# Kernel optimization log

Hardware: AMD Instinct MI355X
Metric: run time of the kernel (lower is better)

## Reference

```python
import jax, jax.numpy as jnp
import numpy as np

ROUTING_ITERS = 3
EPS = 1e-12


def squash(s):
    # squash over both pose-matrix dims (axis=[-2,-1])
    n2 = jnp.sum(s * s, axis=(-2, -1), keepdims=True)
    n = jnp.sqrt(n2 + EPS)
    return s * (n2 / (1.0 + n2)) / n


def setup_inputs() -> dict:
    key = jax.random.key(0)
    k1, k2, k3 = jax.random.split(key, 3)
    B, I, O = 32, 4096, 32
    input_poses = jax.random.normal(k1, (B, I, 4, 4), dtype=jnp.float32)
    input_activations = jax.random.uniform(k2, (B, I), dtype=jnp.float32)
    # weight: [num_capsules, num_input_caps, 4, 4] (trans_in=trans_out=False for 4x4->4x4)
    w = jax.random.normal(k3, (O, I, 4, 4), dtype=jnp.float32) * 0.05
    return {"input_poses": input_poses, "input_activations": input_activations, "w": w}


def reference(input_poses, input_activations, w):
    # votes: expand_dims(poses,1) @ w, broadcast over output capsules -> [B,O,I,4,4]
    votes = jnp.einsum("bixy,oiyz->boixz", input_poses, w)
    B, O, I = votes.shape[0], votes.shape[1], votes.shape[2]

    # dynamic routing (routing-by-agreement)
    b = jnp.zeros((B, O, I), dtype=votes.dtype)
    s = None
    for it in range(ROUTING_ITERS):
        c = jax.nn.softmax(b, axis=1)  # couple over output capsules
        s = jnp.einsum("boi,boixy->boxy", c, votes)  # weighted sum [B,O,4,4]
        if it < ROUTING_ITERS - 1:
            v = squash(s)
            b = b + jnp.einsum("boixy,boxy->boi", votes, v)

    capsule_poses = squash(s)  # activation == 'squash'
    capsule_activations = jnp.sqrt(jnp.sum(capsule_poses * capsule_poses, axis=(-2, -1)) + EPS)
    return capsule_poses, capsule_activations
```

## Files before the change

### kernel.cpp

```cpp
#include <hip/hip_runtime.h>
#include <math.h>


#define NB 32
#define NI 4096
#define NO 32
#define I_TILE 16
#define NCHUNK (NI / I_TILE)
#define B_TILE 8
#define NBG (NB / B_TILE)
#define WSTR_I 578
#define WSTR_O 18
#define SOFF (NB * NO * 16)
#define EPSF 1e-12f

__device__ __forceinline__ float4 row_mm(const float4 p, const float4 w0,
                                         const float4 w1, const float4 w2,
                                         const float4 w3) {
    float4 r;
    r.x = fmaf(p.x, w0.x, fmaf(p.y, w1.x, fmaf(p.z, w2.x, p.w * w3.x)));
    r.y = fmaf(p.x, w0.y, fmaf(p.y, w1.y, fmaf(p.z, w2.y, p.w * w3.y)));
    r.z = fmaf(p.x, w0.z, fmaf(p.y, w1.z, fmaf(p.z, w2.z, p.w * w3.z)));
    r.w = fmaf(p.x, w0.w, fmaf(p.y, w1.w, fmaf(p.z, w2.w, p.w * w3.w)));
    return r;
}

__device__ __forceinline__ float dot4(const float4 a, const float4 b) {
    return fmaf(a.x, b.x, fmaf(a.y, b.y, fmaf(a.z, b.z, a.w * b.w)));
}

__device__ __forceinline__ void fma4(float4& s, const float c, const float4 t) {
    s.x = fmaf(c, t.x, s.x);
    s.y = fmaf(c, t.y, s.y);
    s.z = fmaf(c, t.z, s.z);
    s.w = fmaf(c, t.w, s.w);
}

template <int CTRL>
__device__ __forceinline__ float dpp_add(float x) {
    int xi = __builtin_bit_cast(int, x);
    int yi = __builtin_amdgcn_update_dpp(0, xi, CTRL, 0xf, 0xf, false);
    return x + __builtin_bit_cast(float, yi);
}

__device__ __forceinline__ float sum32(float x) {
    x = dpp_add<0xB1>(x);
    x = dpp_add<0x4E>(x);
    x = dpp_add<0x141>(x);
    x = dpp_add<0x140>(x);
    int t = __builtin_amdgcn_ds_swizzle(__builtin_bit_cast(int, x), 0x401F);
    return x + __builtin_bit_cast(float, t);
}

__global__ __launch_bounds__(256, 4) void caps_pass_st(
    const float* __restrict__ poses, const float* __restrict__ w,
    const float* __restrict__ v_buf, float* __restrict__ s_part,
    const int pass)
{
    __shared__ float wsm[I_TILE * WSTR_I];
    const int tid    = threadIdx.x;
    const int chunk  = blockIdx.x;
    const int bgroup = blockIdx.y;
    const int ibase  = chunk * I_TILE;

    #pragma unroll
    for (int r = 0; r < 8; ++r) {
        const int idx = r * 256 + tid;
        const int o_l = idx >> 6;
        const int rem = idx & 63;
        const int i_l = rem >> 2;
        const int k4  = rem & 3;
        const float4 val = *(const float4*)(
            w + (((size_t)o_l * NI + ibase + i_l) << 4) + (k4 << 2));
        float* dst = &wsm[i_l * WSTR_I + o_l * WSTR_O + (k4 << 2)];
        ((float2*)dst)[0] = make_float2(val.x, val.y);
        ((float2*)dst)[1] = make_float2(val.z, val.w);
    }

    const int o    = tid & 31;
    const int bsub = tid >> 5;
    const int b    = bgroup * B_TILE + bsub;
    const int bo   = b * NO + o;

    float4 vv0 = {0,0,0,0}, vv1 = {0,0,0,0}, vv2 = {0,0,0,0}, vv3 = {0,0,0,0};
    if (pass > 0) {
        const float4* vp = (const float4*)(v_buf + (bo << 4));
        vv0 = vp[0]; vv1 = vp[1]; vv2 = vp[2]; vv3 = vp[3];
    }

    const float*  wrow  = &wsm[o * WSTR_O];
    const float4* pbase = (const float4*)(poses + (((size_t)b * NI + ibase) << 4));

    __syncthreads();

    float4 s0 = {0,0,0,0}, s1 = {0,0,0,0}, s2 = {0,0,0,0}, s3 = {0,0,0,0};

    #pragma unroll 2
    for (int i = 0; i < I_TILE; ++i) {
        const float2* wr = (const float2*)(wrow + i * WSTR_I);
        const float2 a0 = wr[0], a1 = wr[1], a2 = wr[2], a3 = wr[3];
        const float2 a4 = wr[4], a5 = wr[5], a6 = wr[6], a7 = wr[7];
        const float4 w0 = make_float4(a0.x, a0.y, a1.x, a1.y);
        const float4 w1 = make_float4(a2.x, a2.y, a3.x, a3.y);
        const float4 w2 = make_float4(a4.x, a4.y, a5.x, a5.y);
        const float4 w3 = make_float4(a6.x, a6.y, a7.x, a7.y);
        const float4 p0 = pbase[(i << 2) + 0];
        const float4 p1 = pbase[(i << 2) + 1];
        const float4 p2 = pbase[(i << 2) + 2];
        const float4 p3 = pbase[(i << 2) + 3];

        const float4 t0 = row_mm(p0, w0, w1, w2, w3);
        const float4 t1 = row_mm(p1, w0, w1, w2, w3);
        const float4 t2 = row_mm(p2, w0, w1, w2, w3);
        const float4 t3 = row_mm(p3, w0, w1, w2, w3);

        float cc;
        if (pass == 0) {
            cc = 1.0f / 32.0f;
        } else {
            const float d = dot4(t0,vv0) + dot4(t1,vv1)
                          + dot4(t2,vv2) + dot4(t3,vv3);
            const float e  = __expf(d);
            const float es = sum32(e);
            cc = __fdividef(e, es);
        }
        fma4(s0, cc, t0); fma4(s1, cc, t1);
        fma4(s2, cc, t2); fma4(s3, cc, t3);
    }

    float4* sp = (float4*)(s_part + ((size_t)chunk * (NB * NO) + bo) * 16);
    sp[0] = s0; sp[1] = s1; sp[2] = s2; sp[3] = s3;
}

__global__ __launch_bounds__(256) void caps_reduce(
    const float* __restrict__ s_part, float* __restrict__ v_buf,
    float* __restrict__ out, const int pass)
{
    const int e  = threadIdx.x & 63;
    const int c4 = threadIdx.x >> 6;
    const int eg = blockIdx.x * 64 + e;

    float acc = 0.0f;
    #pragma unroll 8
    for (int j = 0; j < NCHUNK / 4; ++j) {
        const int c = c4 * (NCHUNK / 4) + j;
        acc += s_part[(size_t)c * SOFF + eg];
    }
    __shared__ float red[4][64];
    red[c4][e] = acc;
    __syncthreads();

    if (threadIdx.x < 64) {
        const float a = red[0][e] + red[1][e] + red[2][e] + red[3][e];
        float x = a * a;
        #pragma unroll
        for (int msk = 8; msk >= 1; msk >>= 1)
            x += __shfl_xor(x, msk, 16);
        const float n2 = x;
        const float n  = sqrtf(n2 + EPSF);
        const float sc = (n2 / (1.0f + n2)) / n;
        if (pass < 2) {
            const float vold = (pass == 0) ? 0.0f : v_buf[eg];
            v_buf[eg] = fmaf(sc, a, vold);
        } else {
            out[eg] = sc * a;
            if ((e & 15) == 0)
                out[NB * NO * 16 + (eg >> 4)] = sqrtf(n2 * sc * sc + EPSF);
        }
    }
}

#define FB_CHUNKS 32
#define FB_IPB (NI / FB_CHUNKS)

__global__ __launch_bounds__(256) void caps_pass_fb(
    const float* __restrict__ poses, const float* __restrict__ w,
    const float* __restrict__ v_buf, float* __restrict__ s_buf, const int mode)
{
    const int tid   = threadIdx.x;
    const int b     = blockIdx.y;
    const int chunk = blockIdx.x;
    const int o     = tid & 31;
    const int g     = tid >> 5;

    float4 v0 = {0,0,0,0}, v1 = {0,0,0,0}, v2 = {0,0,0,0}, v3 = {0,0,0,0};
    if (mode != 0) {
        const float4* vp = (const float4*)(v_buf + (((b * NO) + o) << 4));
        v0 = vp[0]; v1 = vp[1]; v2 = vp[2]; v3 = vp[3];
    }
    float4 s0 = {0,0,0,0}, s1 = {0,0,0,0}, s2 = {0,0,0,0}, s3 = {0,0,0,0};
    const int ibase = chunk * FB_IPB + g;
    #pragma unroll 4
    for (int it = 0; it < FB_IPB / 8; ++it) {
        const int i = ibase + (it << 3);
        const float4* pp = (const float4*)(poses + ((((size_t)b * NI) + i) << 4));
        const float4 p0 = pp[0], p1 = pp[1], p2 = pp[2], p3 = pp[3];
        const float4* wp = (const float4*)(w + ((((size_t)o * NI) + i) << 4));
        const float4 w0 = wp[0], w1 = wp[1], w2 = wp[2], w3 = wp[3];
        const float4 t0 = row_mm(p0, w0, w1, w2, w3);
        const float4 t1 = row_mm(p1, w0, w1, w2, w3);
        const float4 t2 = row_mm(p2, w0, w1, w2, w3);
        const float4 t3 = row_mm(p3, w0, w1, w2, w3);
        float cc;
        if (mode == 0) {
            cc = 1.0f / 32.0f;
        } else {
            float d = dot4(t0,v0) + dot4(t1,v1) + dot4(t2,v2) + dot4(t3,v3);
            const float e  = __expf(d);
            const float es = sum32(e);
            cc = __fdividef(e, es);
        }
        fma4(s0, cc, t0); fma4(s1, cc, t1);
        fma4(s2, cc, t2); fma4(s3, cc, t3);
    }
    __shared__ float red[8][32][16];
    float4* rp = (float4*)&red[g][o][0];
    rp[0] = s0; rp[1] = s1; rp[2] = s2; rp[3] = s3;
    __syncthreads();
    for (int idx = tid; idx < NO * 16; idx += 256) {
        const int oo = idx >> 4;
        const int k  = idx & 15;
        float acc = red[0][oo][k];
        #pragma unroll
        for (int gg = 1; gg < 8; ++gg) acc += red[gg][oo][k];
        atomicAdd(&s_buf[(((b * NO) + oo) << 4) + k], acc);
    }
}

__global__ __launch_bounds__(256) void caps_squash_fb(
    float* __restrict__ s_buf, float* __restrict__ v_buf,
    float* __restrict__ out, const int mode)
{
    const int idx = blockIdx.x * 256 + threadIdx.x;
    if (idx >= NB * NO) return;
    float4* sp = (float4*)(s_buf + (idx << 4));
    const float4 s0 = sp[0], s1 = sp[1], s2 = sp[2], s3 = sp[3];
    const float n2 = dot4(s0,s0) + dot4(s1,s1) + dot4(s2,s2) + dot4(s3,s3);
    const float n  = sqrtf(n2 + EPSF);
    const float sc = (n2 / (1.0f + n2)) / n;
    if (mode == 2) {
        float4* op = (float4*)(out + (idx << 4));
        op[0] = make_float4(sc*s0.x, sc*s0.y, sc*s0.z, sc*s0.w);
        op[1] = make_float4(sc*s1.x, sc*s1.y, sc*s1.z, sc*s1.w);
        op[2] = make_float4(sc*s2.x, sc*s2.y, sc*s2.z, sc*s2.w);
        op[3] = make_float4(sc*s3.x, sc*s3.y, sc*s3.z, sc*s3.w);
        out[NB * NO * 16 + idx] = sqrtf(n2 * sc * sc + EPSF);
    } else {
        float4* vp = (float4*)(v_buf + (idx << 4));
        float4 a0 = {0,0,0,0}, a1 = {0,0,0,0}, a2 = {0,0,0,0}, a3 = {0,0,0,0};
        if (mode != 0) { a0 = vp[0]; a1 = vp[1]; a2 = vp[2]; a3 = vp[3]; }
        vp[0] = make_float4(fmaf(sc,s0.x,a0.x), fmaf(sc,s0.y,a0.y), fmaf(sc,s0.z,a0.z), fmaf(sc,s0.w,a0.w));
        vp[1] = make_float4(fmaf(sc,s1.x,a1.x), fmaf(sc,s1.y,a1.y), fmaf(sc,s1.z,a1.z), fmaf(sc,s1.w,a1.w));
        vp[2] = make_float4(fmaf(sc,s2.x,a2.x), fmaf(sc,s2.y,a2.y), fmaf(sc,s2.z,a2.z), fmaf(sc,s2.w,a2.w));
        vp[3] = make_float4(fmaf(sc,s3.x,a3.x), fmaf(sc,s3.y,a3.y), fmaf(sc,s3.z,a3.z), fmaf(sc,s3.w,a3.w));
        const float4 z = {0,0,0,0};
        sp[0] = z; sp[1] = z; sp[2] = z; sp[3] = z;
    }
}

extern "C" void kernel_launch(void* const* d_in, const int* in_sizes, int n_in,
                              void* d_out, int out_size, void* d_ws, size_t ws_size,
                              hipStream_t stream) {
    const float* poses = (const float*)d_in[0];
    const float* w     = (const float*)d_in[2];
    float* out = (float*)d_out;

    const size_t need = ((size_t)NCHUNK * SOFF + SOFF) * sizeof(float);
    if (ws_size >= need) {
        float* s_part = (float*)d_ws;
        float* v_buf  = s_part + (size_t)NCHUNK * SOFF;
        dim3 gp(NCHUNK, NBG), blk(256), gr(256);
        for (int pass = 0; pass < 3; ++pass) {
            caps_pass_st<<<gp, blk, 0, stream>>>(poses, w, v_buf, s_part, pass);
            caps_reduce<<<gr, blk, 0, stream>>>(s_part, v_buf, out, pass);
        }
    } else {
        float* s_buf = (float*)d_ws;
        float* v_buf = s_buf + SOFF;
        hipMemsetAsync(s_buf, 0, SOFF * sizeof(float), stream);
        dim3 grid(FB_CHUNKS, NB), block(256);
        for (int pass = 0; pass < 3; ++pass) {
            caps_pass_fb<<<grid, block, 0, stream>>>(poses, w, v_buf, s_buf, pass);
            caps_squash_fb<<<4, 256, 0, stream>>>(s_buf, v_buf, out, pass);
        }
    }
}
```

Measured before the change: 138.5 us.

## Pack poses and weights to fp16 and compute votes with fdot2

Adds a pre-pass kernel that converts poses and weights to fp16 pairs, with the weights transposed for dot2 access. The main routing pass then loads half as many bytes and computes each vote element with two packed fp16 dot-product instructions instead of four fp32 FMAs. The shared-memory weight tile becomes a simpler uint4 layout. This adds a pack launch and extra workspace, loses precision in the votes, and falls back to the fp32 path if the workspace is too small.

```diff
diff --git a/kernel.cpp b/kernel.cpp
--- a/kernel.cpp
+++ b/kernel.cpp
@@ -9,21 +9,20 @@
 #define NCHUNK (NI / I_TILE)
 #define B_TILE 8
 #define NBG (NB / B_TILE)
-#define WSTR_I 578
-#define WSTR_O 18
 #define SOFF (NB * NO * 16)
 #define EPSF 1e-12f
 
-__device__ __forceinline__ float4 row_mm(const float4 p, const float4 w0,
-                                         const float4 w1, const float4 w2,
-                                         const float4 w3) {
-    float4 r;
-    r.x = fmaf(p.x, w0.x, fmaf(p.y, w1.x, fmaf(p.z, w2.x, p.w * w3.x)));
-    r.y = fmaf(p.x, w0.y, fmaf(p.y, w1.y, fmaf(p.z, w2.y, p.w * w3.y)));
-    r.z = fmaf(p.x, w0.z, fmaf(p.y, w1.z, fmaf(p.z, w2.z, p.w * w3.z)));
-    r.w = fmaf(p.x, w0.w, fmaf(p.y, w1.w, fmaf(p.z, w2.w, p.w * w3.w)));
-    return r;
-}
+typedef _Float16 v2h __attribute__((ext_vector_type(2)));
+
+#if __has_builtin(__builtin_amdgcn_fdot2)
+__device__ __forceinline__ float fdot2(v2h a, v2h b, float c) {
+    return __builtin_amdgcn_fdot2(a, b, c, false);
+}
+#else
+__device__ __forceinline__ float fdot2(v2h a, v2h b, float c) {
+    return fmaf((float)a.x, (float)b.x, fmaf((float)a.y, (float)b.y, c));
+}
+#endif
 
 __device__ __forceinline__ float dot4(const float4 a, const float4 b) {
     return fmaf(a.x, b.x, fmaf(a.y, b.y, fmaf(a.z, b.z, a.w * b.w)));
@@ -52,29 +51,68 @@
     return x + __builtin_bit_cast(float, t);
 }
 
+__global__ __launch_bounds__(256) void caps_pack(
+    const float* __restrict__ poses, const float* __restrict__ w,
+    v2h* __restrict__ pp, v2h* __restrict__ wp)
+{
+    const int n = blockIdx.x * 256 + threadIdx.x;
+    if (n >= NO * NI) return;
+    {
+        float Wv[16];
+        const float4* src = (const float4*)(w + ((size_t)n << 4));
+        *(float4*)&Wv[0] = src[0]; *(float4*)&Wv[4]  = src[1];
+        *(float4*)&Wv[8] = src[2]; *(float4*)&Wv[12] = src[3];
+        v2h o8[8];
+        #pragma unroll
+        for (int z = 0; z < 4; ++z) {
+            v2h a, b;
+            a.x = (_Float16)Wv[0 * 4 + z]; a.y = (_Float16)Wv[1 * 4 + z];
+            b.x = (_Float16)Wv[2 * 4 + z]; b.y = (_Float16)Wv[3 * 4 + z];
+            o8[2 * z] = a; o8[2 * z + 1] = b;
+        }
+        uint4* dst = (uint4*)(wp + (size_t)n * 8);
+        dst[0] = *(uint4*)&o8[0];
+        dst[1] = *(uint4*)&o8[4];
+    }
+    {
+        float Pv[16];
+        const float4* src = (const float4*)(poses + ((size_t)n << 4));
+        *(float4*)&Pv[0] = src[0]; *(float4*)&Pv[4]  = src[1];
+        *(float4*)&Pv[8] = src[2]; *(float4*)&Pv[12] = src[3];
+        v2h o8[8];
+        #pragma unroll
+        for (int x = 0; x < 4; ++x) {
+            v2h a, b;
+            a.x = (_Float16)Pv[x * 4 + 0]; a.y = (_Float16)Pv[x * 4 + 1];
+            b.x = (_Float16)Pv[x * 4 + 2]; b.y = (_Float16)Pv[x * 4 + 3];
+            o8[2 * x] = a; o8[2 * x + 1] = b;
+        }
+        uint4* dst = (uint4*)(pp + (size_t)n * 8);
+        dst[0] = *(uint4*)&o8[0];
+        dst[1] = *(uint4*)&o8[4];
+    }
+}
+
 __global__ __launch_bounds__(256, 4) void caps_pass_st(
-    const float* __restrict__ poses, const float* __restrict__ w,
+    const v2h* __restrict__ pp, const v2h* __restrict__ wp,
     const float* __restrict__ v_buf, float* __restrict__ s_part,
     const int pass)
 {
-    __shared__ float wsm[I_TILE * WSTR_I];
+    __shared__ uint4 wsm[I_TILE][32][2];
     const int tid    = threadIdx.x;
     const int chunk  = blockIdx.x;
     const int bgroup = blockIdx.y;
     const int ibase  = chunk * I_TILE;
 
+    const uint4* wpu = (const uint4*)wp;
     #pragma unroll
-    for (int r = 0; r < 8; ++r) {
+    for (int r = 0; r < 4; ++r) {
         const int idx = r * 256 + tid;
-        const int o_l = idx >> 6;
-        const int rem = idx & 63;
-        const int i_l = rem >> 2;
-        const int k4  = rem & 3;
-        const float4 val = *(const float4*)(
-            w + (((size_t)o_l * NI + ibase + i_l) << 4) + (k4 << 2));
-        float* dst = &wsm[i_l * WSTR_I + o_l * WSTR_O + (k4 << 2)];
-        ((float2*)dst)[0] = make_float2(val.x, val.y);
-        ((float2*)dst)[1] = make_float2(val.z, val.w);
+        const int o_l = idx >> 5;
+        const int rem = idx & 31;
+        const int i_l = rem >> 1;
+        const int h   = rem & 1;
+        wsm[i_l][o_l][h] = wpu[((size_t)(o_l * NI + ibase + i_l) << 1) + h];
     }
 
     const int o    = tid & 31;
@@ -88,8 +126,7 @@
         vv0 = vp[0]; vv1 = vp[1]; vv2 = vp[2]; vv3 = vp[3];
     }
 
-    const float*  wrow  = &wsm[o * WSTR_O];
-    const float4* pbase = (const float4*)(poses + (((size_t)b * NI + ibase) << 4));
+    const uint4* ppu = (const uint4*)(pp + ((size_t)(b * NI + ibase) << 3));
 
     __syncthreads();
 
@@ -97,22 +134,32 @@
 
     #pragma unroll 2
     for (int i = 0; i < I_TILE; ++i) {
-        const float2* wr = (const float2*)(wrow + i * WSTR_I);
-        const float2 a0 = wr[0], a1 = wr[1], a2 = wr[2], a3 = wr[3];
-        const float2 a4 = wr[4], a5 = wr[5], a6 = wr[6], a7 = wr[7];
-        const float4 w0 = make_float4(a0.x, a0.y, a1.x, a1.y);
-        const float4 w1 = make_float4(a2.x, a2.y, a3.x, a3.y);
-        const float4 w2 = make_float4(a4.x, a4.y, a5.x, a5.y);
-        const float4 w3 = make_float4(a6.x, a6.y, a7.x, a7.y);
-        const float4 p0 = pbase[(i << 2) + 0];
-        const float4 p1 = pbase[(i << 2) + 1];
-        const float4 p2 = pbase[(i << 2) + 2];
-        const float4 p3 = pbase[(i << 2) + 3];
-
-        const float4 t0 = row_mm(p0, w0, w1, w2, w3);
-        const float4 t1 = row_mm(p1, w0, w1, w2, w3);
-        const float4 t2 = row_mm(p2, w0, w1, w2, w3);
-        const float4 t3 = row_mm(p3, w0, w1, w2, w3);
+        const uint4 pa = ppu[2 * i + 0];
+        const uint4 pb = ppu[2 * i + 1];
+        const uint4 wa = wsm[i][o][0];
+        const uint4 wb = wsm[i][o][1];
+        const v2h* ph0 = (const v2h*)&pa;
+        const v2h* ph1 = (const v2h*)&pb;
+        const v2h* wh0 = (const v2h*)&wa;
+        const v2h* wh1 = (const v2h*)&wb;
+
+        float4 t0, t1, t2, t3;
+        t0.x = fdot2(ph0[0], wh0[0], fdot2(ph0[1], wh0[1], 0.0f));
+        t0.y = fdot2(ph0[0], wh0[2], fdot2(ph0[1], wh0[3], 0.0f));
+        t0.z = fdot2(ph0[0], wh1[0], fdot2(ph0[1], wh1[1], 0.0f));
+        t0.w = fdot2(ph0[0], wh1[2], fdot2(ph0[1], wh1[3], 0.0f));
+        t1.x = fdot2(ph0[2], wh0[0], fdot2(ph0[3], wh0[1], 0.0f));
+        t1.y = fdot2(ph0[2], wh0[2], fdot2(ph0[3], wh0[3], 0.0f));
+        t1.z = fdot2(ph0[2], wh1[0], fdot2(ph0[3], wh1[1], 0.0f));
+        t1.w = fdot2(ph0[2], wh1[2], fdot2(ph0[3], wh1[3], 0.0f));
+        t2.x = fdot2(ph1[0], wh0[0], fdot2(ph1[1], wh0[1], 0.0f));
+        t2.y = fdot2(ph1[0], wh0[2], fdot2(ph1[1], wh0[3], 0.0f));
+        t2.z = fdot2(ph1[0], wh1[0], fdot2(ph1[1], wh1[1], 0.0f));
+        t2.w = fdot2(ph1[0], wh1[2], fdot2(ph1[1], wh1[3], 0.0f));
+        t3.x = fdot2(ph1[2], wh0[0], fdot2(ph1[3], wh0[1], 0.0f));
+        t3.y = fdot2(ph1[2], wh0[2], fdot2(ph1[3], wh0[3], 0.0f));
+        t3.z = fdot2(ph1[2], wh1[0], fdot2(ph1[3], wh1[1], 0.0f));
+        t3.w = fdot2(ph1[2], wh1[2], fdot2(ph1[3], wh1[3], 0.0f));
 
         float cc;
         if (pass == 0) {
@@ -173,6 +220,17 @@
 #define FB_CHUNKS 32
 #define FB_IPB (NI / FB_CHUNKS)
 
+__device__ __forceinline__ float4 row_mm(const float4 p, const float4 w0,
+                                         const float4 w1, const float4 w2,
+                                         const float4 w3) {
+    float4 r;
+    r.x = fmaf(p.x, w0.x, fmaf(p.y, w1.x, fmaf(p.z, w2.x, p.w * w3.x)));
+    r.y = fmaf(p.x, w0.y, fmaf(p.y, w1.y, fmaf(p.z, w2.y, p.w * w3.y)));
+    r.z = fmaf(p.x, w0.z, fmaf(p.y, w1.z, fmaf(p.z, w2.z, p.w * w3.z)));
+    r.w = fmaf(p.x, w0.w, fmaf(p.y, w1.w, fmaf(p.z, w2.w, p.w * w3.w)));
+    return r;
+}
+
 __global__ __launch_bounds__(256) void caps_pass_fb(
     const float* __restrict__ poses, const float* __restrict__ w,
     const float* __restrict__ v_buf, float* __restrict__ s_buf, const int mode)
@@ -193,10 +251,10 @@
     #pragma unroll 4
     for (int it = 0; it < FB_IPB / 8; ++it) {
         const int i = ibase + (it << 3);
-        const float4* pp = (const float4*)(poses + ((((size_t)b * NI) + i) << 4));
-        const float4 p0 = pp[0], p1 = pp[1], p2 = pp[2], p3 = pp[3];
-        const float4* wp = (const float4*)(w + ((((size_t)o * NI) + i) << 4));
-        const float4 w0 = wp[0], w1 = wp[1], w2 = wp[2], w3 = wp[3];
+        const float4* ppf = (const float4*)(poses + ((((size_t)b * NI) + i) << 4));
+        const float4 p0 = ppf[0], p1 = ppf[1], p2 = ppf[2], p3 = ppf[3];
+        const float4* wpf = (const float4*)(w + ((((size_t)o * NI) + i) << 4));
+        const float4 w0 = wpf[0], w1 = wpf[1], w2 = wpf[2], w3 = wpf[3];
         const float4 t0 = row_mm(p0, w0, w1, w2, w3);
         const float4 t1 = row_mm(p1, w0, w1, w2, w3);
         const float4 t2 = row_mm(p2, w0, w1, w2, w3);
@@ -265,13 +323,19 @@
     const float* w     = (const float*)d_in[2];
     float* out = (float*)d_out;
 
-    const size_t need = ((size_t)NCHUNK * SOFF + SOFF) * sizeof(float);
+    const size_t need = ((size_t)NCHUNK * SOFF + SOFF) * sizeof(float)
+                      + (size_t)2 * NO * NI * 8 * sizeof(v2h);
     if (ws_size >= need) {
         float* s_part = (float*)d_ws;
         float* v_buf  = s_part + (size_t)NCHUNK * SOFF;
+        v2h*   pp     = (v2h*)(v_buf + SOFF);
+        v2h*   wp     = pp + (size_t)NO * NI * 8;
+
+        caps_pack<<<(NO * NI + 255) / 256, 256, 0, stream>>>(poses, w, pp, wp);
+
         dim3 gp(NCHUNK, NBG), blk(256), gr(256);
         for (int pass = 0; pass < 3; ++pass) {
-            caps_pass_st<<<gp, blk, 0, stream>>>(poses, w, v_buf, s_part, pass);
+            caps_pass_st<<<gp, blk, 0, stream>>>(pp, wp, v_buf, s_part, pass);
             caps_reduce<<<gr, blk, 0, stream>>>(s_part, v_buf, out, pass);
         }
     } else {
```

Result: no change. 140.8 us (+1.7%).
